# Kernel optimization log

Hardware: AMD Instinct MI355X
Metric: run time of the kernel (lower is better)

Reference implementation:

```python
import jax, jax.numpy as jnp
import numpy as np

T, S, F = 256, 128, 1024  # t frames, s persons, person_feature_len (= attn_len)


def setup_inputs() -> dict:
    key = jax.random.key(0)
    ks = jax.random.split(key, 9)
    scale = 1.0 / np.sqrt(F)
    return {
        "batch_data": jax.random.normal(ks[0], (T * S, F), dtype=jnp.float32),
        "xywh": jax.random.uniform(ks[1], (T * S, 4), dtype=jnp.float32),
        "Wa": jax.random.normal(ks[2], (F, F), dtype=jnp.float32) * scale,
        "ba": jnp.zeros((F,), dtype=jnp.float32),
        "Wb": jax.random.normal(ks[3], (F, F), dtype=jnp.float32) * scale,
        "bb": jnp.zeros((F,), dtype=jnp.float32),
        "Wg": jax.random.normal(ks[4], (F, F), dtype=jnp.float32) * scale,
        "bg": jnp.zeros((F,), dtype=jnp.float32),
        "OW": 1280,
        "OH": 720,
        "num_person": jax.random.randint(ks[5], (T,), 0, S, dtype=jnp.int64),
    }


def reference(batch_data, xywh, Wa, ba, Wb, bb, Wg, bg, OW, OH, num_person):
    # SemPosBlock.forward: only the SpatioVisualModule path contributes to the output.
    x = batch_data.reshape(T, S, F)            # person features per frame
    theta = jnp.einsum("tsf,fa->tsa", x, Wa) + ba
    phi = jnp.einsum("tsf,fa->tsa", x, Wb) + bb
    feats = jnp.einsum("tsf,fa->tsa", x, Wg) + bg
    # per-frame person-person attention: softmax(theta @ phi^T) @ feats
    scores = jnp.einsum("tsa,tja->tsj", theta, phi)     # [T, S, S]
    weights = jax.nn.softmax(scores, axis=-1)
    results = jnp.einsum("tsj,tja->tsa", weights, feats)  # [T, S, F]
    return results
```

## Files before the change

kernel.cpp:

```cpp
#include <hip/hip_runtime.h>

typedef _Float16 f16x8 __attribute__((ext_vector_type(8)));
typedef __attribute__((ext_vector_type(4))) float f32x4;

__device__ __forceinline__ unsigned short f16b(float x){
  _Float16 h = (_Float16)x;
  return __builtin_bit_cast(unsigned short, h);
}
__device__ __forceinline__ void split2h(float x, unsigned short &hi, unsigned short &lo){
  _Float16 h = (_Float16)x;
  _Float16 l = (_Float16)(x - (float)h);
  hi = __builtin_bit_cast(unsigned short, h);
  lo = __builtin_bit_cast(unsigned short, l);
}
__device__ __forceinline__ void gload_lds16(const void* g, void* l){
  __builtin_amdgcn_global_load_lds((const __attribute__((address_space(1))) void*)g,
                                   (__attribute__((address_space(3))) void*)l, 16, 0, 0);
}
#define VM(N)    asm volatile("s_waitcnt vmcnt(" #N ")" ::: "memory")
#define LGKM0()  do { asm volatile("s_waitcnt lgkmcnt(0)" ::: "memory"); \
                      __builtin_amdgcn_sched_barrier(0); } while(0)
#define BAR()    do { __builtin_amdgcn_s_barrier(); \
                      __builtin_amdgcn_sched_barrier(0); } while(0)

template<int MAP>
__device__ __forceinline__ int kmap(int k){
  if (MAP == 1) return (k < 2048) ? k : (k - 2048);
  if (MAP == 2) return (k < 1024) ? k : (k - 1024);
  if (MAP == 3) return k & 1023;
  return k;
}

template<int MAPA, int MAPB, int NK, int EPI>
__device__ __forceinline__ void gemm_body(
    const unsigned short* __restrict__ A, const unsigned short* __restrict__ B,
    unsigned short* __restrict__ outp, const float* __restrict__ bias,
    int lda, int ldb, int bm, int bn, char* ldsb)
{
  const int tid  = threadIdx.x;
  const int w    = tid >> 6;
  const int lane = tid & 63;
  const int wm   = w >> 2;
  const int wn   = w & 3;
  const int l15  = lane & 15;
  const int lg   = lane >> 4;

  int srow[2], slg[2];
#pragma unroll
  for (int j = 0; j < 2; j++){
    int o16 = j * 512 + tid;
    int p = o16 >> 3, s = o16 & 7;
    int q = s ^ (p & 7);
    srow[j] = 2 * p + (q >> 2);
    slg[j]  = q & 3;
  }
  const unsigned short* aS0 = A + (size_t)(bm * 256 + srow[0]) * lda + slg[0] * 8;
  const unsigned short* aS1 = A + (size_t)(bm * 256 + srow[1]) * lda + slg[1] * 8;
  const unsigned short* bS0 = B + (size_t)(bn * 256 + srow[0]) * ldb + slg[0] * 8;
  const unsigned short* bS1 = B + (size_t)(bn * 256 + srow[1]) * ldb + slg[1] * 8;

  const int sA   = (((l15 & 1) << 2) | lg) ^ ((l15 >> 1) & 7);
  const int rps  = (l15 >> 1) * 128 + sA * 16;

  f32x4 acc[8][4];
  f32x4 zero = {0.f, 0.f, 0.f, 0.f};
#pragma unroll
  for (int m = 0; m < 8; m++)
#pragma unroll
    for (int n = 0; n < 4; n++) acc[m][n] = zero;

  auto STAGE_Q = [&](int t, int q){
    char* slot = ldsb + (size_t)(t & 1) * 65536;
    const int kbA = kmap<MAPA>(t * 64);
    const int kbB = kmap<MAPB>(t * 64);
    if (q == 0){
      gload_lds16(aS0 + kbA,      slot +         w * 1024);
      gload_lds16(aS1 + kbA,      slot +  8192 + w * 1024);
    } else if (q == 1){
      gload_lds16(bS0 + kbB,      slot + 32768 + w * 1024);
      gload_lds16(bS1 + kbB,      slot + 40960 + w * 1024);
    } else if (q == 2){
      gload_lds16(bS0 + kbB + 32, slot + 49152 + w * 1024);
      gload_lds16(bS1 + kbB + 32, slot + 57344 + w * 1024);
    } else {
      gload_lds16(aS0 + kbA + 32, slot + 16384 + w * 1024);
      gload_lds16(aS1 + kbA + 32, slot + 24576 + w * 1024);
    }
  };

  STAGE_Q(0, 0); STAGE_Q(0, 1); STAGE_Q(0, 2); STAGE_Q(0, 3);

#pragma unroll 1
  for (int t = 0; t < NK; t++){
    const char* sb = ldsb + (size_t)(t & 1) * 65536;
    const bool pre = (t + 1 < NK);
    f16x8 aF[4], bF[4], aG[4], bF2[4], aF2[4], aG2[4];

    VM(4);
    BAR();
    if (pre) STAGE_Q(t + 1, 0);
#pragma unroll
    for (int m = 0; m < 4; m++) aF[m] = *(const f16x8*)(sb + wm * 8192 + m * 1024 + rps);
#pragma unroll
    for (int n = 0; n < 4; n++) bF[n] = *(const f16x8*)(sb + 32768 + wn * 4096 + n * 1024 + rps);
    LGKM0();
    __builtin_amdgcn_s_setprio(1);
#pragma unroll
    for (int m = 0; m < 4; m++)
#pragma unroll
      for (int n = 0; n < 4; n++)
        acc[m][n] = __builtin_amdgcn_mfma_f32_16x16x32_f16(aF[m], bF[n], acc[m][n], 0, 0, 0);
    __builtin_amdgcn_s_setprio(0);
    if (pre) STAGE_Q(t + 1, 1);
#pragma unroll
    for (int m = 0; m < 4; m++) aG[m] = *(const f16x8*)(sb + wm * 8192 + (m + 4) * 1024 + rps);
    LGKM0();
    __builtin_amdgcn_s_setprio(1);
#pragma unroll
    for (int m = 0; m < 4; m++)
#pragma unroll
      for (int n = 0; n < 4; n++)
        acc[m + 4][n] = __builtin_amdgcn_mfma_f32_16x16x32_f16(aG[m], bF[n], acc[m + 4][n], 0, 0, 0);
    __builtin_amdgcn_s_setprio(0);

    if (pre) { VM(4); } else { VM(0); }
    BAR();
    if (pre) STAGE_Q(t + 1, 2);
#pragma unroll
    for (int m = 0; m < 4; m++) aF2[m] = *(const f16x8*)(sb + 16384 + wm * 8192 + m * 1024 + rps);
#pragma unroll
    for (int n = 0; n < 4; n++) bF2[n] = *(const f16x8*)(sb + 49152 + wn * 4096 + n * 1024 + rps);
    LGKM0();
    __builtin_amdgcn_s_setprio(1);
#pragma unroll
    for (int m = 0; m < 4; m++)
#pragma unroll
      for (int n = 0; n < 4; n++)
        acc[m][n] = __builtin_amdgcn_mfma_f32_16x16x32_f16(aF2[m], bF2[n], acc[m][n], 0, 0, 0);
    __builtin_amdgcn_s_setprio(0);
    if (pre) STAGE_Q(t + 1, 3);
#pragma unroll
    for (int m = 0; m < 4; m++) aG2[m] = *(const f16x8*)(sb + 16384 + wm * 8192 + (m + 4) * 1024 + rps);
    LGKM0();
    __builtin_amdgcn_s_setprio(1);
#pragma unroll
    for (int m = 0; m < 4; m++)
#pragma unroll
      for (int n = 0; n < 4; n++)
        acc[m + 4][n] = __builtin_amdgcn_mfma_f32_16x16x32_f16(aG2[m], bF2[n], acc[m + 4][n], 0, 0, 0);
    __builtin_amdgcn_s_setprio(0);
  }

#pragma unroll
  for (int m = 0; m < 8; m++)
#pragma unroll
    for (int n = 0; n < 4; n++){
      const int col  = bn * 256 + wn * 64 + n * 16 + l15;
      const int row0 = bm * 256 + wm * 128 + m * 16 + lg * 4;
      if (EPI == 1){
        const float bgv = bias[col];
        ushort4 h4;
        h4.x = f16b(acc[m][n][0] + bgv); h4.y = f16b(acc[m][n][1] + bgv);
        h4.z = f16b(acc[m][n][2] + bgv); h4.w = f16b(acc[m][n][3] + bgv);
        *(ushort4*)(outp + (size_t)col * 32768 + row0) = h4;
      } else if (EPI == 4){
#pragma unroll
        for (int q = 0; q < 4; q++)
          outp[(size_t)(row0 + q) * 2048 + col] = f16b(acc[m][n][q]);
      } else if (EPI == 6){
        float* of = (float*)outp;
#pragma unroll
        for (int q = 0; q < 4; q++)
          of[(size_t)col * 1024 + row0 + q] = acc[m][n][q];
      }
    }
}

template<int MAPA, int MAPB, int NK, int EPI>
__global__ __launch_bounds__(512, 2) void k_gemm256(
    const unsigned short* __restrict__ A, const unsigned short* __restrict__ B,
    unsigned short* __restrict__ outp, const float* __restrict__ bias,
    int lda, int ldb)
{
  __shared__ __align__(16) unsigned short lds_u[65536];
  int bid = blockIdx.x;
  bid = (bid & 7) * (gridDim.x >> 3) + (bid >> 3);
  gemm_body<MAPA, MAPB, NK, EPI>(A, B, outp, bias, lda, ldb, bid >> 2, bid & 3, (char*)lds_u);
}

__global__ __launch_bounds__(512, 1) void k_mtx(
    const unsigned short* __restrict__ Wa2, const unsigned short* __restrict__ Wb2,
    float* __restrict__ Mpart,
    const float* __restrict__ x, unsigned short* __restrict__ x2,
    const float* __restrict__ wv, float* __restrict__ v)
{
  __shared__ __align__(16) unsigned short lds_u[65536];
  const int b = blockIdx.x;
  if (b < 96){
    const int s = b >> 5, rest = b & 31;
    const int kc = rest >> 4, tile = rest & 15;
    const unsigned short* Aa = Wa2 + (s == 1 ? 1024 : 0) + kc * 512;
    const unsigned short* Bb = Wb2 + (s == 2 ? 1024 : 0) + kc * 512;
    gemm_body<0, 0, 8, 6>(Aa, Bb, (unsigned short*)(Mpart + (size_t)(s * 2 + kc) * 1048576),
                          nullptr, 2048, 2048, tile >> 2, tile & 3, (char*)lds_u);
  } else {
    const int bb = b - 96;
    const int w = threadIdx.x >> 6, lane = threadIdx.x & 63;
#pragma unroll
    for (int it = 0; it < 4; it++){
      const int row = bb * 8 + w + it * 8192;
      float s = 0.f;
#pragma unroll
      for (int j = 0; j < 4; j++){
        const int c = lane * 4 + j * 256;
        float4 val = *(const float4*)(x + (size_t)row * 1024 + c);
        float4 wvv = *(const float4*)(wv + c);
        ushort4 h, l;
        split2h(val.x, h.x, l.x); split2h(val.y, h.y, l.y);
        split2h(val.z, h.z, l.z); split2h(val.w, h.w, l.w);
        *(ushort4*)(x2 + (size_t)row * 2048 + c) = h;
        *(ushort4*)(x2 + (size_t)row * 2048 + 1024 + c) = l;
        s += val.x * wvv.x + val.y * wvv.y + val.z * wvv.z + val.w * wvv.w;
      }
      for (int o = 32; o; o >>= 1) s += __shfl_xor(s, o);
      if (lane == 0) v[row] = s;
    }
  }
}

__global__ __launch_bounds__(256) void k_mt_reduce(const float* __restrict__ P,
                                                   unsigned short* __restrict__ MTh){
  const size_t i = ((size_t)blockIdx.x * 256 + threadIdx.x) * 4;
  float4 s = *(const float4*)(P + i);
#pragma unroll
  for (int p = 1; p < 6; p++){
    float4 a = *(const float4*)(P + (size_t)p * 1048576 + i);
    s.x += a.x; s.y += a.y; s.z += a.z; s.w += a.w;
  }
  ushort4 h;
  h.x = f16b(s.x); h.y = f16b(s.y); h.z = f16b(s.z); h.w = f16b(s.w);
  *(ushort4*)(MTh + i) = h;
}

__global__ __launch_bounds__(1024) void k_frame(
    const unsigned short* Y2, const unsigned short* X2,
    const float* __restrict__ v, const unsigned short* __restrict__ FT,
    float* outp)
{
  __shared__ __align__(16) unsigned short lds_u[65536];
  char* ldsb = (char*)lds_u;

  const int frame = blockIdx.x;
  const int tid  = threadIdx.x;
  const int w    = tid >> 6;
  const int lane = tid & 63;
  const int wm   = w >> 2;
  const int wn   = w & 3;
  const int l15  = lane & 15;
  const int lg   = lane >> 4;

  const int cS = tid & 511, hS = tid >> 9;
  const int pS = cS >> 3, sS = cS & 7;
  const int qS = sS ^ (pS & 7);
  const int srow = 2 * pS + (qS >> 2);
  const int slg  = qS & 3;
  const unsigned short* yS = Y2 + (size_t)(frame * 128 + srow) * 2048 + slg * 8;
  const unsigned short* xS = X2 + (size_t)(frame * 128 + srow) * 2048 + slg * 8;
  const int dY  =         hS * 8192 + cS * 16;
  const int dXh = 16384 + hS * 8192 + cS * 16;
  const int dXl = 32768 + hS * 8192 + cS * 16;

  const int sA  = (((l15 & 1) << 2) | lg) ^ ((l15 >> 1) & 7);
  const int rps = (l15 >> 1) * 128 + sA * 16;

  f32x4 acc[2][2];
  f32x4 zero = {0.f, 0.f, 0.f, 0.f};
#pragma unroll
  for (int m = 0; m < 2; m++)
#pragma unroll
    for (int n = 0; n < 2; n++) acc[m][n] = zero;

  auto STAGE_K = [&](int t){
    char* slot = ldsb + (size_t)(t & 1) * 49152;
    const int kk = t * 64 + hS * 32;
    gload_lds16(yS + kk,        slot + dY);
    gload_lds16(xS + kk,        slot + dXh);
    gload_lds16(xS + 1024 + kk, slot + dXl);
  };

  const int NK = 16;
  STAGE_K(0);

#pragma unroll 1
  for (int t = 0; t < NK; t++){
    const char* sb = ldsb + (size_t)(t & 1) * 49152;
    if (t + 1 < NK){ STAGE_K(t + 1); VM(3); } else { VM(0); }
    BAR();
    f16x8 aF[2][2], bh[2][2], bl[2][2];
#pragma unroll
    for (int h = 0; h < 2; h++){
#pragma unroll
      for (int m = 0; m < 2; m++)
        aF[h][m] = *(const f16x8*)(sb + h * 8192 + (wm * 2 + m) * 1024 + rps);
#pragma unroll
      for (int n = 0; n < 2; n++)
        bh[h][n] = *(const f16x8*)(sb + 16384 + h * 8192 + (wn * 2 + n) * 1024 + rps);
#pragma unroll
      for (int n = 0; n < 2; n++)
        bl[h][n] = *(const f16x8*)(sb + 32768 + h * 8192 + (wn * 2 + n) * 1024 + rps);
    }
    LGKM0();
    __builtin_amdgcn_s_setprio(1);
#pragma unroll
    for (int h = 0; h < 2; h++)
#pragma unroll
      for (int m = 0; m < 2; m++)
#pragma unroll
        for (int n = 0; n < 2; n++){
          acc[m][n] = __builtin_amdgcn_mfma_f32_16x16x32_f16(aF[h][m], bh[h][n], acc[m][n], 0, 0, 0);
          acc[m][n] = __builtin_amdgcn_mfma_f32_16x16x32_f16(aF[h][m], bl[h][n], acc[m][n], 0, 0, 0);
        }
    __builtin_amdgcn_s_setprio(0);
    BAR();
  }

  BAR();
  float* sf = (float*)ldsb;
#pragma unroll
  for (int m = 0; m < 2; m++)
#pragma unroll
    for (int n = 0; n < 2; n++){
      const int col = wn * 32 + n * 16 + l15;
#pragma unroll
      for (int q = 0; q < 4; q++){
        const int row = wm * 32 + m * 16 + lg * 4 + q;
        sf[row * 128 + ((col + (row & 31) * 4) & 127)] = acc[m][n][q];
      }
    }
  LGKM0(); BAR();
  unsigned short* Pb = (unsigned short*)(ldsb + 98304);
  {
    const float* vr = v + (size_t)frame * 128;
#pragma unroll 1
    for (int i = 0; i < 8; i++){
      const int row = w * 8 + i;
      const float* rp = sf + row * 128;
      const int rot = (row & 31) * 4;
      float a = rp[(lane + rot) & 127]      + vr[lane];
      float b = rp[(lane + 64 + rot) & 127] + vr[lane + 64];
      float mx = fmaxf(a, b);
      for (int o = 32; o; o >>= 1) mx = fmaxf(mx, __shfl_xor(mx, o));
      float ea = __expf(a - mx), eb = __expf(b - mx);
      float s = ea + eb;
      for (int o = 32; o; o >>= 1) s += __shfl_xor(s, o);
      const float inv = 1.0f / s;
      unsigned short* prow = (unsigned short*)((char*)Pb + row * 256);
      const int j0 = lane, j1 = lane + 64;
      *(unsigned short*)((char*)prow + (((j0 >> 3) ^ (row & 15)) * 16) + (j0 & 7) * 2) = f16b(ea * inv);
      *(unsigned short*)((char*)prow + (((j1 >> 3) ^ (row & 15)) * 16) + (j1 & 7) * 2) = f16b(eb * inv);
    }
  }
  LGKM0(); BAR();

  char* Fb = ldsb;
  auto STAGE_F = [&](int h){
    char* slot = Fb + (size_t)(h & 1) * 32768;
#pragma unroll
    for (int j = 0; j < 2; j++){
      const int o = j * 1024 + tid;
      const int a = o >> 4, c = o & 15;
      gload_lds16(FT + (size_t)(h * 128 + a) * 32768 + frame * 128 + (c ^ (a & 15)) * 8,
                  slot + (size_t)o * 16);
    }
  };
  STAGE_F(0);

#pragma unroll 1
  for (int h = 0; h < 8; h++){
    if (h + 1 < 8){ STAGE_F(h + 1); VM(2); } else { VM(0); }
    BAR();
    const char* fs = Fb + (size_t)(h & 1) * 32768;
    f16x8 pF[4][2], fF[4][2];
#pragma unroll
    for (int ks = 0; ks < 4; ks++){
#pragma unroll
      for (int m = 0; m < 2; m++){
        const int row = wm * 32 + m * 16 + l15;
        pF[ks][m] = *(const f16x8*)((char*)Pb + row * 256 + (((ks * 4 + lg) ^ (row & 15)) * 16));
      }
#pragma unroll
      for (int n = 0; n < 2; n++){
        const int al = wn * 32 + n * 16 + l15;
        fF[ks][n] = *(const f16x8*)(fs + al * 256 + (((ks * 4 + lg) ^ (al & 15)) * 16));
      }
    }
    LGKM0();
    f32x4 accP[2][2];
#pragma unroll
    for (int m = 0; m < 2; m++)
#pragma unroll
      for (int n = 0; n < 2; n++) accP[m][n] = zero;
    __builtin_amdgcn_s_setprio(1);
#pragma unroll
    for (int ks = 0; ks < 4; ks++)
#pragma unroll
      for (int m = 0; m < 2; m++)
#pragma unroll
        for (int n = 0; n < 2; n++)
          accP[m][n] = __builtin_amdgcn_mfma_f32_16x16x32_f16(pF[ks][m], fF[ks][n], accP[m][n], 0, 0, 0);
    __builtin_amdgcn_s_setprio(0);
#pragma unroll
    for (int m = 0; m < 2; m++)
#pragma unroll
      for (int n = 0; n < 2; n++){
        const int f  = h * 128 + wn * 32 + n * 16 + l15;
        const int r0 = wm * 32 + m * 16 + lg * 4;
#pragma unroll
        for (int q = 0; q < 4; q++)
          outp[((size_t)frame * 128 + r0 + q) * 1024 + f] = accP[m][n][q];
      }
    BAR();
  }
}

__global__ __launch_bounds__(256) void k_prep(const float* __restrict__ Wa,
                                              const float* __restrict__ Wb,
                                              const float* __restrict__ Wg,
                                              const float* __restrict__ ba,
                                              unsigned short* __restrict__ Wa2,
                                              unsigned short* __restrict__ Wb2,
                                              unsigned short* __restrict__ WgTh,
                                              float* __restrict__ wv){
  const int b = blockIdx.x;
  if (b < 2048){
    const int row = (b < 1024) ? b : (b - 1024);
    const float* src = (b < 1024) ? Wa : Wb;
    unsigned short* dst = (b < 1024) ? Wa2 : Wb2;
    const int c = threadIdx.x * 4;
    float4 val = *(const float4*)(src + (size_t)row * 1024 + c);
    ushort4 h, l;
    split2h(val.x, h.x, l.x); split2h(val.y, h.y, l.y);
    split2h(val.z, h.z, l.z); split2h(val.w, h.w, l.w);
    *(ushort4*)(dst + (size_t)row * 2048 + c) = h;
    *(ushort4*)(dst + (size_t)row * 2048 + 1024 + c) = l;
  } else if (b < 3072){
    const int row = b - 2048;
    const int c0 = threadIdx.x * 4;
    float4 val = *(const float4*)(Wg + (size_t)row * 1024 + c0);
    float vv[4] = {val.x, val.y, val.z, val.w};
#pragma unroll
    for (int i = 0; i < 4; i++)
      WgTh[(size_t)(c0 + i) * 1024 + row] = f16b(vv[i]);
  } else {
    const int row = (b - 3072) * 4 + (threadIdx.x >> 6);
    const int lane = threadIdx.x & 63;
    float s = 0.f;
#pragma unroll
    for (int j = 0; j < 4; j++){
      const int c = lane * 4 + j * 256;
      float4 wb = *(const float4*)(Wb + (size_t)row * 1024 + c);
      float4 bb = *(const float4*)(ba + c);
      s += wb.x * bb.x + wb.y * bb.y + wb.z * bb.z + wb.w * bb.w;
    }
    for (int o = 32; o; o >>= 1) s += __shfl_xor(s, o);
    if (lane == 0) wv[row] = s;
  }
}

extern "C" void kernel_launch(void* const* d_in, const int* in_sizes, int n_in,
                              void* d_out, int out_size, void* d_ws, size_t ws_size,
                              hipStream_t stream) {
  const float* x  = (const float*)d_in[0];
  const float* Wa = (const float*)d_in[2];
  const float* ba = (const float*)d_in[3];
  const float* Wb = (const float*)d_in[4];
  const float* Wg = (const float*)d_in[6];
  const float* bg = (const float*)d_in[7];

  unsigned short* x2   = (unsigned short*)d_ws;
  unsigned short* Wa2  = x2 + (size_t)32768 * 2048;
  unsigned short* Wb2  = Wa2 + (size_t)1024 * 2048;
  unsigned short* WgTh = Wb2 + (size_t)1024 * 2048;
  unsigned short* MTh  = WgTh + (size_t)1024 * 1024;
  unsigned short* FT   = MTh + (size_t)1024 * 1024;
  float* Mpart = (float*)(FT + (size_t)1024 * 32768);
  float* wv = Mpart + (size_t)6 * 1048576;
  float* v  = wv + 1024;
  size_t need = (size_t)((char*)(v + 32768) - (char*)d_ws);
  if (ws_size < need) return;

  unsigned short* y2 = (unsigned short*)d_out;

  k_prep      <<<3328, 256, 0, stream>>>(Wa, Wb, Wg, ba, Wa2, Wb2, WgTh, wv);
  k_mtx       <<<1120, 512, 0, stream>>>(Wa2, Wb2, Mpart, x, x2, wv, v);
  k_gemm256<0, 0, 16, 1><<<512, 512, 0, stream>>>(x2, WgTh, FT, bg, 2048, 1024);
  k_mt_reduce <<<1024, 256, 0, stream>>>(Mpart, MTh);
  k_gemm256<0, 0, 16, 4><<<512, 512, 0, stream>>>(x2, MTh, y2, nullptr, 2048, 1024);
  k_frame     <<<256, 1024, 0, stream>>>(y2, x2, v, FT, (float*)d_out);
}
```

Measured before the change: 314.2 us.

## Drop fp16 low-split of x and merge the two big GEMMs into one launch

Stores x as a single fp16 copy instead of a hi/lo split pair, halving the x2 write and read traffic and removing the extra low-part MFMAs in the per-frame score GEMM. The two large GEMMs, x·M^T and the Wg projection, now run as two halves of one 1024-block launch. That removes a launch and lets them overlap. The Wg GEMM is reoriented with a new epilogue that adds the bias per row. Accuracy drops because the fp16 residual correction of x is gone, which may affect tolerance.

```diff
diff --git a/kernel.cpp b/kernel.cpp
--- a/kernel.cpp
+++ b/kernel.cpp
@@ -24,12 +24,7 @@
                       __builtin_amdgcn_sched_barrier(0); } while(0)
 
 template<int MAP>
-__device__ __forceinline__ int kmap(int k){
-  if (MAP == 1) return (k < 2048) ? k : (k - 2048);
-  if (MAP == 2) return (k < 1024) ? k : (k - 1024);
-  if (MAP == 3) return k & 1023;
-  return k;
-}
+__device__ __forceinline__ int kmap(int k){ return k; }
 
 template<int MAPA, int MAPB, int NK, int EPI>
 __device__ __forceinline__ void gemm_body(
@@ -157,13 +152,7 @@
     for (int n = 0; n < 4; n++){
       const int col  = bn * 256 + wn * 64 + n * 16 + l15;
       const int row0 = bm * 256 + wm * 128 + m * 16 + lg * 4;
-      if (EPI == 1){
-        const float bgv = bias[col];
-        ushort4 h4;
-        h4.x = f16b(acc[m][n][0] + bgv); h4.y = f16b(acc[m][n][1] + bgv);
-        h4.z = f16b(acc[m][n][2] + bgv); h4.w = f16b(acc[m][n][3] + bgv);
-        *(ushort4*)(outp + (size_t)col * 32768 + row0) = h4;
-      } else if (EPI == 4){
+      if (EPI == 4){
 #pragma unroll
         for (int q = 0; q < 4; q++)
           outp[(size_t)(row0 + q) * 2048 + col] = f16b(acc[m][n][q]);
@@ -172,20 +161,29 @@
 #pragma unroll
         for (int q = 0; q < 4; q++)
           of[(size_t)col * 1024 + row0 + q] = acc[m][n][q];
-      }
-    }
-}
-
-template<int MAPA, int MAPB, int NK, int EPI>
-__global__ __launch_bounds__(512, 2) void k_gemm256(
-    const unsigned short* __restrict__ A, const unsigned short* __restrict__ B,
-    unsigned short* __restrict__ outp, const float* __restrict__ bias,
-    int lda, int ldb)
+      } else if (EPI == 7){
+#pragma unroll
+        for (int q = 0; q < 4; q++)
+          outp[(size_t)(row0 + q) * 32768 + col] = f16b(acc[m][n][q] + bias[row0 + q]);
+      }
+    }
+}
+
+__global__ __launch_bounds__(512, 2) void k_big(
+    const unsigned short* __restrict__ x2, const unsigned short* __restrict__ MTh,
+    unsigned short* __restrict__ y2, const unsigned short* __restrict__ WgTh,
+    unsigned short* __restrict__ FT, const float* __restrict__ bg)
 {
   __shared__ __align__(16) unsigned short lds_u[65536];
-  int bid = blockIdx.x;
-  bid = (bid & 7) * (gridDim.x >> 3) + (bid >> 3);
-  gemm_body<MAPA, MAPB, NK, EPI>(A, B, outp, bias, lda, ldb, bid >> 2, bid & 3, (char*)lds_u);
+  const int b = blockIdx.x;
+  if (b < 512){
+    int bid = (b & 7) * 64 + (b >> 3);
+    gemm_body<0, 0, 16, 4>(x2, MTh, y2, nullptr, 1024, 1024, bid >> 2, bid & 3, (char*)lds_u);
+  } else {
+    int fb = b - 512;
+    int fbid = (fb & 7) * 64 + (fb >> 3);
+    gemm_body<0, 0, 16, 7>(WgTh, x2, FT, bg, 1024, 1024, fbid >> 7, fbid & 127, (char*)lds_u);
+  }
 }
 
 __global__ __launch_bounds__(512, 1) void k_mtx(
@@ -218,8 +216,7 @@
         ushort4 h, l;
         split2h(val.x, h.x, l.x); split2h(val.y, h.y, l.y);
         split2h(val.z, h.z, l.z); split2h(val.w, h.w, l.w);
-        *(ushort4*)(x2 + (size_t)row * 2048 + c) = h;
-        *(ushort4*)(x2 + (size_t)row * 2048 + 1024 + c) = l;
+        *(ushort4*)(x2 + (size_t)row * 1024 + c) = h;
         s += val.x * wvv.x + val.y * wvv.y + val.z * wvv.z + val.w * wvv.w;
       }
       for (int o = 32; o; o >>= 1) s += __shfl_xor(s, o);
@@ -247,7 +244,7 @@
     const float* __restrict__ v, const unsigned short* __restrict__ FT,
     float* outp)
 {
-  __shared__ __align__(16) unsigned short lds_u[65536];
+  __shared__ __align__(16) unsigned short lds_u[49152];
   char* ldsb = (char*)lds_u;
 
   const int frame = blockIdx.x;
@@ -265,10 +262,9 @@
   const int srow = 2 * pS + (qS >> 2);
   const int slg  = qS & 3;
   const unsigned short* yS = Y2 + (size_t)(frame * 128 + srow) * 2048 + slg * 8;
-  const unsigned short* xS = X2 + (size_t)(frame * 128 + srow) * 2048 + slg * 8;
-  const int dY  =         hS * 8192 + cS * 16;
-  const int dXh = 16384 + hS * 8192 + cS * 16;
-  const int dXl = 32768 + hS * 8192 + cS * 16;
+  const unsigned short* xS = X2 + (size_t)(frame * 128 + srow) * 1024 + slg * 8;
+  const int dY =         hS * 8192 + cS * 16;
+  const int dX = 16384 + hS * 8192 + cS * 16;
 
   const int sA  = (((l15 & 1) << 2) | lg) ^ ((l15 >> 1) & 7);
   const int rps = (l15 >> 1) * 128 + sA * 16;
@@ -281,11 +277,10 @@
     for (int n = 0; n < 2; n++) acc[m][n] = zero;
 
   auto STAGE_K = [&](int t){
-    char* slot = ldsb + (size_t)(t & 1) * 49152;
+    char* slot = ldsb + (size_t)(t & 1) * 32768;
     const int kk = t * 64 + hS * 32;
-    gload_lds16(yS + kk,        slot + dY);
-    gload_lds16(xS + kk,        slot + dXh);
-    gload_lds16(xS + 1024 + kk, slot + dXl);
+    gload_lds16(yS + kk, slot + dY);
+    gload_lds16(xS + kk, slot + dX);
   };
 
   const int NK = 16;
@@ -293,10 +288,10 @@
 
 #pragma unroll 1
   for (int t = 0; t < NK; t++){
-    const char* sb = ldsb + (size_t)(t & 1) * 49152;
-    if (t + 1 < NK){ STAGE_K(t + 1); VM(3); } else { VM(0); }
-    BAR();
-    f16x8 aF[2][2], bh[2][2], bl[2][2];
+    const char* sb = ldsb + (size_t)(t & 1) * 32768;
+    if (t + 1 < NK){ STAGE_K(t + 1); VM(2); } else { VM(0); }
+    BAR();
+    f16x8 aF[2][2], bh[2][2];
 #pragma unroll
     for (int h = 0; h < 2; h++){
 #pragma unroll
@@ -305,9 +300,6 @@
 #pragma unroll
       for (int n = 0; n < 2; n++)
         bh[h][n] = *(const f16x8*)(sb + 16384 + h * 8192 + (wn * 2 + n) * 1024 + rps);
-#pragma unroll
-      for (int n = 0; n < 2; n++)
-        bl[h][n] = *(const f16x8*)(sb + 32768 + h * 8192 + (wn * 2 + n) * 1024 + rps);
     }
     LGKM0();
     __builtin_amdgcn_s_setprio(1);
@@ -316,10 +308,8 @@
 #pragma unroll
       for (int m = 0; m < 2; m++)
 #pragma unroll
-        for (int n = 0; n < 2; n++){
+        for (int n = 0; n < 2; n++)
           acc[m][n] = __builtin_amdgcn_mfma_f32_16x16x32_f16(aF[h][m], bh[h][n], acc[m][n], 0, 0, 0);
-          acc[m][n] = __builtin_amdgcn_mfma_f32_16x16x32_f16(aF[h][m], bl[h][n], acc[m][n], 0, 0, 0);
-        }
     __builtin_amdgcn_s_setprio(0);
     BAR();
   }
@@ -338,7 +328,7 @@
       }
     }
   LGKM0(); BAR();
-  unsigned short* Pb = (unsigned short*)(ldsb + 98304);
+  unsigned short* Pb = (unsigned short*)(ldsb + 65536);
   {
     const float* vr = v + (size_t)frame * 128;
 #pragma unroll 1
@@ -478,7 +468,7 @@
   const float* bg = (const float*)d_in[7];
 
   unsigned short* x2   = (unsigned short*)d_ws;
-  unsigned short* Wa2  = x2 + (size_t)32768 * 2048;
+  unsigned short* Wa2  = x2 + (size_t)32768 * 1024;
   unsigned short* Wb2  = Wa2 + (size_t)1024 * 2048;
   unsigned short* WgTh = Wb2 + (size_t)1024 * 2048;
   unsigned short* MTh  = WgTh + (size_t)1024 * 1024;
@@ -493,8 +483,7 @@
 
   k_prep      <<<3328, 256, 0, stream>>>(Wa, Wb, Wg, ba, Wa2, Wb2, WgTh, wv);
   k_mtx       <<<1120, 512, 0, stream>>>(Wa2, Wb2, Mpart, x, x2, wv, v);
-  k_gemm256<0, 0, 16, 1><<<512, 512, 0, stream>>>(x2, WgTh, FT, bg, 2048, 1024);
   k_mt_reduce <<<1024, 256, 0, stream>>>(Mpart, MTh);
-  k_gemm256<0, 0, 16, 4><<<512, 512, 0, stream>>>(x2, MTh, y2, nullptr, 2048, 1024);
+  k_big       <<<1024, 512, 0, stream>>>(x2, MTh, y2, WgTh, FT, bg);
   k_frame     <<<256, 1024, 0, stream>>>(y2, x2, v, FT, (float*)d_out);
 }
```

Result: faster. 282.1 us (-10.2%).
